# Optimization experiments

Measured on AMD Instinct MI355X. Metric: run time of the kernel, lower is better.

The kernel has to match this reference:

```python
import jax, jax.numpy as jnp
import numpy as np

TOPK = 2  # config.topk_exp


def setup_inputs() -> dict:
    key = jax.random.key(0)
    ks = jax.random.split(key, 4)
    B, S, D, F, E = 4, 1024, 768, 3072, 8
    scale_in = 1.0 / np.sqrt(D)
    scale_hid = 1.0 / np.sqrt(F)
    return {
        "x": jax.random.normal(ks[0], (B, S, D), dtype=jnp.float32),
        "router_w": jax.random.normal(ks[1], (E, D), dtype=jnp.float32) * scale_in,
        "w_fc": jax.random.normal(ks[2], (E, D, F), dtype=jnp.float32) * scale_in,
        "b_fc": jnp.zeros((E, F), dtype=jnp.float32),
        "w_proj": jax.random.normal(ks[3], (E, F, D), dtype=jnp.float32) * scale_hid,
        "b_proj": jnp.zeros((E, D), dtype=jnp.float32),
    }


def _moe_forward(x, router_w, w_fc, b_fc, w_proj, b_proj):
    B, S, D = x.shape
    E = router_w.shape[0]
    xt = x.reshape(-1, D)  # [T, D] tokens
    # per-token router: Linear(D, E, bias=False)
    gate_logits = xt @ router_w.T  # [T, E]
    # topk_exp > 1: raw logits -> topk -> softmax over the k selected logits
    weights, selected = jax.lax.top_k(gate_logits, TOPK)  # [T, k]
    weights = jax.nn.softmax(weights.astype(jnp.float32), axis=1).astype(x.dtype)
    # combine weights per expert: w[t, e] = sum_k weights[t,k] * (selected[t,k]==e)
    onehot = jax.nn.one_hot(selected, E, dtype=x.dtype)  # [T, k, E]
    comb = jnp.einsum('tk,tke->te', weights, onehot)  # [T, E]
    # expert MLP (GPT-2 style: fc -> gelu -> proj), evaluated densely then combined
    h = jax.nn.gelu(jnp.einsum('td,edf->etf', xt, w_fc) + b_fc[:, None, :], approximate=False)
    y = jnp.einsum('etf,efd->etd', h, w_proj) + b_proj[:, None, :]  # [E, T, D]
    out = jnp.einsum('te,etd->td', comb, y)  # weighted scatter-combine
    return out.reshape(B, S, D)


def reference(x, router_w, w_fc, b_fc, w_proj, b_proj):
    return _moe_forward(x, router_w, w_fc, b_fc, w_proj, b_proj)
```

## Files before the change

kernel.cpp:

```cpp
#include <hip/hip_runtime.h>
#include <hip/hip_bf16.h>

#define TT 4096
#define DD 768
#define FF 3072
#define EE 8
#define NSLOT 8192
#define NSLOT_PAD 8448

#define WVM0  0x0F70

typedef __attribute__((ext_vector_type(8))) short bf16x8;
typedef __attribute__((ext_vector_type(4))) float f32x4;
typedef const __attribute__((address_space(1))) void* gas1_t;
typedef __attribute__((address_space(3))) void* las3_t;

__global__ __launch_bounds__(256) void router2_kernel(const float* __restrict__ x,
    const float* __restrict__ rw, int* __restrict__ tokE, float* __restrict__ tokW,
    int* __restrict__ blkCnt) {
  __shared__ float rws[EE * 832];
  __shared__ int cnt_s[EE];
  int tid = threadIdx.x;
  if (tid < EE) cnt_s[tid] = 0;
#pragma unroll
  for (int k = 0; k < 6; ++k) {
    int c = tid + k * 256;
    int e = c / 192, rem = c % 192;
    int s = rem / 12, i = rem % 12;
    float4 v = *(const float4*)&rw[e * DD + s * 48 + i * 4];
    *(float4*)&rws[e * 832 + s * 52 + i * 4] = v;
  }
  __syncthreads();
  int lane = tid & 63;
  int sl = lane & 15;
  int t = blockIdx.x * 16 + (tid >> 6) * 4 + (lane >> 4);
  const float4* xp = (const float4*)(x + (size_t)t * DD + sl * 48);
  float acc[EE];
#pragma unroll
  for (int e = 0; e < EE; ++e) acc[e] = 0.f;
#pragma unroll
  for (int i = 0; i < 12; ++i) {
    float4 xv = xp[i];
#pragma unroll
    for (int e = 0; e < EE; ++e) {
      float4 rv = *(const float4*)&rws[e * 832 + sl * 52 + i * 4];
      acc[e] = fmaf(xv.x, rv.x, fmaf(xv.y, rv.y, fmaf(xv.z, rv.z, fmaf(xv.w, rv.w, acc[e]))));
    }
  }
#pragma unroll
  for (int off = 8; off > 0; off >>= 1) {
#pragma unroll
    for (int e = 0; e < EE; ++e) acc[e] += __shfl_xor(acc[e], off);
  }
  if (sl == 0) {
    float v0 = -1e30f; int e0 = 0;
#pragma unroll
    for (int e = 0; e < EE; ++e) { if (acc[e] > v0) { v0 = acc[e]; e0 = e; } }
    float v1 = -1e30f; int e1 = 0;
#pragma unroll
    for (int e = 0; e < EE; ++e) { if (e != e0 && acc[e] > v1) { v1 = acc[e]; e1 = e; } }
    float w1 = 1.f / (1.f + __expf(v0 - v1));
    float w0 = 1.f - w1;
    tokE[2 * t] = e0; tokE[2 * t + 1] = e1;
    tokW[2 * t] = w0; tokW[2 * t + 1] = w1;
    atomicAdd(&cnt_s[e0], 1);
    atomicAdd(&cnt_s[e1], 1);
  }
  __syncthreads();
  if (tid < EE) blkCnt[blockIdx.x * EE + tid] = cnt_s[tid];
}

__global__ __launch_bounds__(256) void offsets2_kernel(const int* __restrict__ blkCnt,
    int* __restrict__ offs, int* __restrict__ blkBase,
    int* __restrict__ tile1, int* __restrict__ tile2, int* __restrict__ meta) {
  __shared__ int wsum[4][EE];
  int tid = threadIdx.x;
  int lane = tid & 63, w = tid >> 6;
  int c[EE], s[EE];
#pragma unroll
  for (int e = 0; e < EE; ++e) { c[e] = blkCnt[tid * EE + e]; s[e] = c[e]; }
#pragma unroll
  for (int off = 1; off < 64; off <<= 1) {
#pragma unroll
    for (int e = 0; e < EE; ++e) {
      int v = __shfl_up(s[e], off);
      if (lane >= off) s[e] += v;
    }
  }
  if (lane == 63) {
#pragma unroll
    for (int e = 0; e < EE; ++e) wsum[w][e] = s[e];
  }
  __syncthreads();
#pragma unroll
  for (int e = 0; e < EE; ++e) {
    int pre = 0;
    for (int w2 = 0; w2 < w; ++w2) pre += wsum[w2][e];
    s[e] += pre;
  }
  int tot[EE];
#pragma unroll
  for (int e = 0; e < EE; ++e) tot[e] = wsum[0][e] + wsum[1][e] + wsum[2][e] + wsum[3][e];
  int offl[EE + 1];
  offl[0] = 0;
#pragma unroll
  for (int e = 0; e < EE; ++e) offl[e + 1] = offl[e] + tot[e];
#pragma unroll
  for (int e = 0; e < EE; ++e) blkBase[tid * EE + e] = offl[e] + s[e] - c[e];
  if (tid == 0) {
    for (int e = 0; e <= EE; ++e) offs[e] = offl[e];
    int n1 = 0, n2 = 0;
    for (int e = 0; e < EE; ++e) { n1 += (tot[e] + 127) / 128; n2 += (tot[e] + 255) / 256; }
    meta[0] = n1; meta[1] = n2;
  }
  if (tid < EE) {
    int p1 = 0, p2 = 0;
    for (int e = 0; e < tid; ++e) { p1 += (tot[e] + 127) / 128; p2 += (tot[e] + 255) / 256; }
    for (int m = 0; m < tot[tid]; m += 128) tile1[p1++] = (tid << 20) | m;
    for (int m = 0; m < tot[tid]; m += 256) tile2[p2++] = (tid << 20) | m;
  }
}

__global__ __launch_bounds__(256) void scatter_gather2_kernel(const float* __restrict__ x,
    const int* __restrict__ tokE, const float* __restrict__ tokW,
    const int* __restrict__ blkBase, int* __restrict__ slotIdx, float* __restrict__ slotW,
    int* __restrict__ slotTok, __hip_bfloat16* __restrict__ Xg) {
  __shared__ int base_s[EE], lcur[EE];
  __shared__ int sl_s[16][2];
  int tid = threadIdx.x;
  int b = blockIdx.x;
  if (tid < EE) { base_s[tid] = blkBase[b * EE + tid]; lcur[tid] = 0; }
  __syncthreads();
  if (tid < 16) {
    int t = b * 16 + tid;
    int e0 = tokE[2 * t], e1 = tokE[2 * t + 1];
    int s0 = base_s[e0] + atomicAdd(&lcur[e0], 1);
    int s1 = base_s[e1] + atomicAdd(&lcur[e1], 1);
    slotIdx[2 * t] = s0; slotIdx[2 * t + 1] = s1;
    slotW[s0] = tokW[2 * t]; slotW[s1] = tokW[2 * t + 1];
    slotTok[s0] = t; slotTok[s1] = t;
    sl_s[tid][0] = s0; sl_s[tid][1] = s1;
  }
  __syncthreads();
  int k = tid >> 4, p = tid & 15;
  int t = b * 16 + k;
  int s0 = sl_s[k][0], s1 = sl_s[k][1];
  const float4* src = (const float4*)(x + (size_t)t * DD);
  ushort4* d0 = (ushort4*)(Xg + (size_t)s0 * DD);
  ushort4* d1 = (ushort4*)(Xg + (size_t)s1 * DD);
#pragma unroll
  for (int i = 0; i < 12; ++i) {
    int idx = i * 16 + p;
    float4 v = src[idx];
    union { ushort4 u; __hip_bfloat16 h[4]; } cv;
    cv.h[0] = __float2bfloat16(v.x);
    cv.h[1] = __float2bfloat16(v.y);
    cv.h[2] = __float2bfloat16(v.z);
    cv.h[3] = __float2bfloat16(v.w);
    d0[idx] = cv.u;
    d1[idx] = cv.u;
  }
}

__global__ void transpose_convert_kernel(const float* __restrict__ w_fc, __hip_bfloat16* __restrict__ wfcT,
                                         const float* __restrict__ w_proj, __hip_bfloat16* __restrict__ wprojT) {
  __shared__ float tile[64][65];
  int bx = blockIdx.x;
  const float* S; __hip_bfloat16* D; int K, N, n0, k0;
  if (bx < 576) { S = w_fc;   D = wfcT;   K = DD; N = FF; n0 = (bx % 48) * 64; k0 = (bx / 48) * 64; }
  else { bx -= 576; S = w_proj; D = wprojT; K = FF; N = DD; n0 = (bx % 12) * 64; k0 = (bx / 12) * 64; }
  S += (size_t)blockIdx.z * K * N;
  D += (size_t)blockIdx.z * K * N;
  int tid = threadIdx.x;
#pragma unroll
  for (int i = 0; i < 4; ++i) {
    int slot = i * 256 + tid;
    int r = slot >> 4, c4 = slot & 15;
    float4 v = *(const float4*)&S[(size_t)(k0 + r) * N + n0 + c4 * 4];
    tile[r][c4 * 4 + 0] = v.x; tile[r][c4 * 4 + 1] = v.y;
    tile[r][c4 * 4 + 2] = v.z; tile[r][c4 * 4 + 3] = v.w;
  }
  __syncthreads();
#pragma unroll
  for (int i = 0; i < 4; ++i) {
    int slot = i * 256 + tid;
    int n = slot >> 4, kc = slot & 15;
    union { ushort4 u; __hip_bfloat16 h[4]; } cv;
    cv.h[0] = __float2bfloat16(tile[kc * 4 + 0][n]);
    cv.h[1] = __float2bfloat16(tile[kc * 4 + 1][n]);
    cv.h[2] = __float2bfloat16(tile[kc * 4 + 2][n]);
    cv.h[3] = __float2bfloat16(tile[kc * 4 + 3][n]);
    *(ushort4*)&D[(size_t)(n0 + n) * K + k0 + kc * 4] = cv.u;
  }
}

__device__ __forceinline__ float rcp_fast(float x) {
  float r; asm("v_rcp_f32 %0, %1" : "=v"(r) : "v"(x)); return r;
}

__device__ __forceinline__ float gelu_f(float v) {
  float z = v * 0.70710678118654752f;
  float az = fabsf(z);
  float t = rcp_fast(1.0f + 0.3275911f * az);
  float poly = t * (0.254829592f + t * (-0.284496736f + t * (1.421413741f +
               t * (-1.453152027f + t * 1.061405429f))));
  float erf_abs = 1.0f - poly * __expf(-az * az);
  float erf = copysignf(erf_abs, z);
  return 0.5f * v * (1.0f + erf);
}

#define G_ISSUE(NXT) \
  _Pragma("unroll") for (int i = 0; i < 4; ++i) { \
    __builtin_amdgcn_global_load_lds((gas1_t)gA[i], (las3_t)(&As[NXT][0] + fsd[i]), 16, 0, 0); \
    __builtin_amdgcn_global_load_lds((gas1_t)gB[i], (las3_t)(&Bs[NXT][0] + fsd[i]), 16, 0, 0); \
    gA[i] += 64; gB[i] += 64; }

#define G_COMP(CUR) \
  { const short* cA = &As[CUR][0]; const short* cB = &Bs[CUR][0]; \
    _Pragma("unroll") for (int s = 0; s < 2; ++s) { \
      bf16x8 af[4], bfr[4]; \
      _Pragma("unroll") for (int mi = 0; mi < 4; ++mi) af[mi] = *(const bf16x8*)(cA + (aoff[mi] ^ (s * 32))); \
      _Pragma("unroll") for (int ni = 0; ni < 4; ++ni) bfr[ni] = *(const bf16x8*)(cB + (boff[ni] ^ (s * 32))); \
      _Pragma("unroll") for (int mi = 0; mi < 4; ++mi) \
        _Pragma("unroll") for (int ni = 0; ni < 4; ++ni) \
          acc[mi][ni] = __builtin_amdgcn_mfma_f32_16x16x32_bf16(af[mi], bfr[ni], acc[mi][ni], 0, 0, 0); } }

#define S_MAIN(CUR, NXT) \
  __builtin_amdgcn_s_waitcnt(WVM0); \
  __builtin_amdgcn_s_barrier(); \
  G_ISSUE(NXT) \
  G_COMP(CUR)

#define S_LAST(CUR) \
  __builtin_amdgcn_s_waitcnt(WVM0); \
  __builtin_amdgcn_s_barrier(); \
  G_COMP(CUR)

__global__ __launch_bounds__(256) void gemm2_kernel(const __hip_bfloat16* __restrict__ H,
    const __hip_bfloat16* __restrict__ wprojT, const float* __restrict__ b_proj,
    const float* __restrict__ slotW, const int* __restrict__ slotTok,
    float* __restrict__ out, const int* __restrict__ offs,
    const int* __restrict__ tile1, const int* __restrict__ meta) {
  __shared__ __align__(16) short As[2][128 * 64];
  __shared__ __align__(16) short Bs[2][128 * 64];
  int wg = blockIdx.x + 6 * blockIdx.y;
  int wl = (wg & 7) * 54 + (wg >> 3);
  int bx = wl % 6;
  int by = wl / 6;
  if (by >= meta[0]) return;
  int tv = tile1[by];
  int e = tv >> 20;
  int m_base = tv & 0xFFFFF;
  int off_e = offs[e];
  int n_e = offs[e + 1] - off_e;
  int n0 = bx * 128;
  const short* A = (const short*)H + (size_t)(off_e + m_base) * FF;
  const short* B = (const short*)wprojT + (size_t)e * DD * FF + (size_t)n0 * FF;
  int tid = threadIdx.x;
  int lane = tid & 63, wid = tid >> 6;
  int l15 = lane & 15, q = lane >> 4;
  int wm = wid & 1, wn = wid >> 1;
  int fsd[4];
  const short* gA[4];
  const short* gB[4];
#pragma unroll
  for (int i = 0; i < 4; ++i) {
    int fs = tid + i * 256;
    int m = fs >> 3, c = (fs & 7) ^ (m & 7);
    fsd[i] = fs * 8;
    gA[i] = A + (size_t)m * FF + c * 8;
    gB[i] = B + (size_t)m * FF + c * 8;
  }
  int aoff[4], boff[4];
#pragma unroll
  for (int mi = 0; mi < 4; ++mi) {
    int r = wm * 64 + mi * 16 + l15;
    aoff[mi] = r * 64 + ((q ^ (r & 7)) * 8);
  }
#pragma unroll
  for (int ni = 0; ni < 4; ++ni) {
    int r = wn * 64 + ni * 16 + l15;
    boff[ni] = r * 64 + ((q ^ (r & 7)) * 8);
  }
  f32x4 acc[4][4] = {};
  G_ISSUE(0)
  for (int g = 0; g < 23; ++g) {
    S_MAIN(0, 1)
    S_MAIN(1, 0)
  }
  S_MAIN(0, 1)
  S_LAST(1)
  float bias[4];
#pragma unroll
  for (int ni = 0; ni < 4; ++ni)
    bias[ni] = b_proj[e * DD + n0 + wn * 64 + ni * 16 + l15];
#pragma unroll
  for (int mi = 0; mi < 4; ++mi) {
#pragma unroll
    for (int r = 0; r < 4; ++r) {
      int ml = wm * 64 + mi * 16 + q * 4 + r;
      if (m_base + ml < n_e) {
        int slot = off_e + m_base + ml;
        float w = slotW[slot];
        int tok = slotTok[slot];
        float* op = out + (size_t)tok * DD + n0 + wn * 64;
#pragma unroll
        for (int ni = 0; ni < 4; ++ni)
          atomicAdd(&op[ni * 16 + l15], w * (acc[mi][ni][r] + bias[ni]));
      }
    }
  }
}

#define G1_ISSUE(NXT) \
  _Pragma("unroll") for (int i = 0; i < 4; ++i) { \
    __builtin_amdgcn_global_load_lds((gas1_t)gA[i], (las3_t)(&As[NXT][0] + fsd[i]), 16, 0, 0); \
    __builtin_amdgcn_global_load_lds((gas1_t)gB[i], (las3_t)(&Bs[NXT][0] + fsd[i]), 16, 0, 0); \
    gA[i] += 64; gB[i] += 64; }

#define G1_COMP(CUR) \
  { const short* cA = &As[CUR][0]; const short* cB = &Bs[CUR][0]; \
    _Pragma("unroll") for (int s = 0; s < 2; ++s) { \
      bf16x8 af[8], bfr[4]; \
      _Pragma("unroll") for (int mi = 0; mi < 8; ++mi) af[mi] = *(const bf16x8*)(cA + (aoff[mi] ^ (s * 32))); \
      _Pragma("unroll") for (int ni = 0; ni < 4; ++ni) bfr[ni] = *(const bf16x8*)(cB + (boff[ni] ^ (s * 32))); \
      _Pragma("unroll") for (int mi = 0; mi < 8; ++mi) \
        _Pragma("unroll") for (int ni = 0; ni < 4; ++ni) \
          acc[mi][ni] = __builtin_amdgcn_mfma_f32_16x16x32_bf16(af[mi], bfr[ni], acc[mi][ni], 0, 0, 0); } }

#define S1_MAIN(CUR, NXT) \
  __builtin_amdgcn_s_waitcnt(WVM0); \
  __builtin_amdgcn_s_barrier(); \
  G1_ISSUE(NXT) \
  G1_COMP(CUR)

#define S1_LAST(CUR) \
  __builtin_amdgcn_s_waitcnt(WVM0); \
  __builtin_amdgcn_s_barrier(); \
  G1_COMP(CUR)

__global__ __launch_bounds__(512, 2) void gemm1_kernel(const __hip_bfloat16* __restrict__ Xg,
    const __hip_bfloat16* __restrict__ wfcT, const float* __restrict__ b_fc,
    __hip_bfloat16* __restrict__ H, const int* __restrict__ offs,
    const int* __restrict__ tile2, const int* __restrict__ meta) {
  __shared__ __align__(16) short As[2][256 * 64];
  __shared__ __align__(16) short Bs[2][256 * 64];
  int wg = blockIdx.x + 12 * blockIdx.y;
  int wl = (wg & 7) * 60 + (wg >> 3);
  int bx = wl % 12;
  int by = wl / 12;
  if (by >= meta[1]) return;
  int tv = tile2[by];
  int e = tv >> 20;
  int m_base = tv & 0xFFFFF;
  int off_e = offs[e];
  int n_e = offs[e + 1] - off_e;
  int n0 = bx * 256;
  const short* A = (const short*)Xg + (size_t)(off_e + m_base) * DD;
  const short* B = (const short*)wfcT + (size_t)e * FF * DD + (size_t)n0 * DD;
  int tid = threadIdx.x;
  int lane = tid & 63, wid = tid >> 6;
  int l15 = lane & 15, q = lane >> 4;
  int wm = wid & 1, wn = wid >> 1;
  int fsd[4];
  const short* gA[4];
  const short* gB[4];
#pragma unroll
  for (int i = 0; i < 4; ++i) {
    int fs = tid + i * 512;
    int m = fs >> 3, c = (fs & 7) ^ (m & 7);
    fsd[i] = fs * 8;
    gA[i] = A + (size_t)m * DD + c * 8;
    gB[i] = B + (size_t)m * DD + c * 8;
  }
  int aoff[8], boff[4];
#pragma unroll
  for (int mi = 0; mi < 8; ++mi) {
    int r = wm * 128 + mi * 16 + l15;
    aoff[mi] = r * 64 + ((q ^ (r & 7)) * 8);
  }
#pragma unroll
  for (int ni = 0; ni < 4; ++ni) {
    int r = wn * 64 + ni * 16 + l15;
    boff[ni] = r * 64 + ((q ^ (r & 7)) * 8);
  }
  f32x4 acc[8][4] = {};
  G1_ISSUE(0)
  for (int g = 0; g < 5; ++g) {
    S1_MAIN(0, 1)
    S1_MAIN(1, 0)
  }
  S1_MAIN(0, 1)
  S1_LAST(1)
  float bias[4];
#pragma unroll
  for (int ni = 0; ni < 4; ++ni) bias[ni] = b_fc[e * FF + n0 + wn * 64 + ni * 16 + l15];
  __hip_bfloat16* Hp = H + (size_t)(off_e + m_base) * FF + n0;
#pragma unroll
  for (int mi = 0; mi < 8; ++mi) {
#pragma unroll
    for (int r = 0; r < 4; ++r) {
      int ml = wm * 128 + mi * 16 + q * 4 + r;
      if (m_base + ml < n_e) {
#pragma unroll
        for (int ni = 0; ni < 4; ++ni) {
          int nl = wn * 64 + ni * 16 + l15;
          float v = acc[mi][ni][r] + bias[ni];
          Hp[(size_t)ml * FF + nl] = __float2bfloat16(gelu_f(v));
        }
      }
    }
  }
}

extern "C" void kernel_launch(void* const* d_in, const int* in_sizes, int n_in,
                              void* d_out, int out_size, void* d_ws, size_t ws_size,
                              hipStream_t stream) {
  const float* x        = (const float*)d_in[0];
  const float* router_w = (const float*)d_in[1];
  const float* w_fc     = (const float*)d_in[2];
  const float* b_fc     = (const float*)d_in[3];
  const float* w_proj   = (const float*)d_in[4];
  const float* b_proj   = (const float*)d_in[5];
  float* out = (float*)d_out;

  char* p = (char*)d_ws;
  auto alloc = [&](size_t bytes) {
    char* r = p;
    p += (bytes + 255) & ~(size_t)255;
    return r;
  };
  __hip_bfloat16* wfcT   = (__hip_bfloat16*)alloc((size_t)EE * FF * DD * 2);
  __hip_bfloat16* wprojT = (__hip_bfloat16*)alloc((size_t)EE * DD * FF * 2);
  __hip_bfloat16* Xg     = (__hip_bfloat16*)alloc((size_t)NSLOT_PAD * DD * 2);
  __hip_bfloat16* H      = (__hip_bfloat16*)alloc((size_t)NSLOT_PAD * FF * 2);
  int*   tokE    = (int*)alloc(TT * 2 * 4);
  float* tokW    = (float*)alloc(TT * 2 * 4);
  int*   slotIdx = (int*)alloc(TT * 2 * 4);
  float* slotW   = (float*)alloc(NSLOT_PAD * 4);
  int*   slotTok = (int*)alloc(NSLOT_PAD * 4);
  int*   blkCnt  = (int*)alloc(256 * EE * 4);
  int*   blkBase = (int*)alloc(256 * EE * 4);
  int*   tile1   = (int*)alloc(128 * 4);
  int*   tile2   = (int*)alloc(256 * 4);
  int*   offs    = (int*)alloc(64);
  int*   meta    = (int*)alloc(64);

  hipMemsetAsync(out, 0, (size_t)out_size * 4, stream);
  router2_kernel<<<256, 256, 0, stream>>>(x, router_w, tokE, tokW, blkCnt);
  offsets2_kernel<<<1, 256, 0, stream>>>(blkCnt, offs, blkBase, tile1, tile2, meta);
  scatter_gather2_kernel<<<256, 256, 0, stream>>>(x, tokE, tokW, blkBase, slotIdx, slotW, slotTok, Xg);
  transpose_convert_kernel<<<dim3(1152, 1, EE), 256, 0, stream>>>(w_fc, wfcT, w_proj, wprojT);
  gemm1_kernel<<<dim3(12, 40), 512, 0, stream>>>(Xg, wfcT, b_fc, H, offs, tile2, meta);
  gemm2_kernel<<<dim3(6, 72), 256, 0, stream>>>(H, wprojT, b_proj, slotW, slotTok, out, offs, tile1, meta);
}
```

Baseline: 340.8 us.

## Interleave gemm1 global-to-LDS loads with MFMA phases using barriers and priority

Restructures the gemm1 main loop into four sub-phases per K tile. Each phase loads a slice of A/B fragments from LDS and issues part of the next tile's global_load_lds, then runs a 4x4 MFMA block under raised wave priority, with barriers around each phase. The aim is to spread memory issue across compute and coordinate waves so the matrix cores stay busier, in the style of ping-pong scheduling. In exchange it adds barriers per tile and reorders register use, which may add sync overhead or change register pressure.

```diff
diff --git a/kernel.cpp b/kernel.cpp
--- a/kernel.cpp
+++ b/kernel.cpp
@@ -9,6 +9,7 @@
 #define NSLOT_PAD 8448
 
 #define WVM0  0x0F70
+#define WLG0  0xC07F
 
 typedef __attribute__((ext_vector_type(8))) short bf16x8;
 typedef __attribute__((ext_vector_type(4))) float f32x4;
@@ -312,32 +313,58 @@
   }
 }
 
-#define G1_ISSUE(NXT) \
-  _Pragma("unroll") for (int i = 0; i < 4; ++i) { \
-    __builtin_amdgcn_global_load_lds((gas1_t)gA[i], (las3_t)(&As[NXT][0] + fsd[i]), 16, 0, 0); \
-    __builtin_amdgcn_global_load_lds((gas1_t)gB[i], (las3_t)(&Bs[NXT][0] + fsd[i]), 16, 0, 0); \
-    gA[i] += 64; gB[i] += 64; }
-
-#define G1_COMP(CUR) \
-  { const short* cA = &As[CUR][0]; const short* cB = &Bs[CUR][0]; \
-    _Pragma("unroll") for (int s = 0; s < 2; ++s) { \
-      bf16x8 af[8], bfr[4]; \
-      _Pragma("unroll") for (int mi = 0; mi < 8; ++mi) af[mi] = *(const bf16x8*)(cA + (aoff[mi] ^ (s * 32))); \
-      _Pragma("unroll") for (int ni = 0; ni < 4; ++ni) bfr[ni] = *(const bf16x8*)(cB + (boff[ni] ^ (s * 32))); \
-      _Pragma("unroll") for (int mi = 0; mi < 8; ++mi) \
-        _Pragma("unroll") for (int ni = 0; ni < 4; ++ni) \
-          acc[mi][ni] = __builtin_amdgcn_mfma_f32_16x16x32_bf16(af[mi], bfr[ni], acc[mi][ni], 0, 0, 0); } }
-
-#define S1_MAIN(CUR, NXT) \
-  __builtin_amdgcn_s_waitcnt(WVM0); \
+#define GL1(SRC, ARR, NXT, IDX) \
+  __builtin_amdgcn_global_load_lds((gas1_t)(SRC), (las3_t)(&ARR[NXT][0] + fsd[IDX]), 16, 0, 0);
+
+#define PH_SYNC \
   __builtin_amdgcn_s_barrier(); \
-  G1_ISSUE(NXT) \
-  G1_COMP(CUR)
-
-#define S1_LAST(CUR) \
-  __builtin_amdgcn_s_waitcnt(WVM0); \
-  __builtin_amdgcn_s_barrier(); \
-  G1_COMP(CUR)
+  __builtin_amdgcn_s_waitcnt(WLG0); \
+  __builtin_amdgcn_s_setprio(1);
+
+#define PH_END \
+  __builtin_amdgcn_s_setprio(0); \
+  __builtin_amdgcn_s_barrier();
+
+#define TILE1(CUR, NXT, STG) \
+ { const short* cA = &As[CUR][0]; const short* cB = &Bs[CUR][0]; \
+   bf16x8 b0[4], b1[4], afr[4]; \
+    \
+   _Pragma("unroll") for (int i = 0; i < 4; ++i) afr[i] = *(const bf16x8*)(cA + aoff[i]); \
+   _Pragma("unroll") for (int i = 0; i < 4; ++i) b0[i]  = *(const bf16x8*)(cB + boff[i]); \
+   if (STG) { GL1(gA[0], As, NXT, 0) GL1(gA[1], As, NXT, 1) GL1(gB[0], Bs, NXT, 0) } \
+   PH_SYNC \
+   _Pragma("unroll") for (int mi = 0; mi < 4; ++mi) \
+     _Pragma("unroll") for (int ni = 0; ni < 4; ++ni) \
+       acc[mi][ni] = __builtin_amdgcn_mfma_f32_16x16x32_bf16(afr[mi], b0[ni], acc[mi][ni], 0, 0, 0); \
+   PH_END \
+    \
+   _Pragma("unroll") for (int i = 0; i < 4; ++i) afr[i] = *(const bf16x8*)(cA + (aoff[i] ^ 32)); \
+   _Pragma("unroll") for (int i = 0; i < 4; ++i) b1[i]  = *(const bf16x8*)(cB + (boff[i] ^ 32)); \
+   if (STG) { GL1(gA[2], As, NXT, 2) GL1(gA[3], As, NXT, 3) GL1(gB[1], Bs, NXT, 1) } \
+   PH_SYNC \
+   _Pragma("unroll") for (int mi = 0; mi < 4; ++mi) \
+     _Pragma("unroll") for (int ni = 0; ni < 4; ++ni) \
+       acc[mi][ni] = __builtin_amdgcn_mfma_f32_16x16x32_bf16(afr[mi], b1[ni], acc[mi][ni], 0, 0, 0); \
+   PH_END \
+    \
+   _Pragma("unroll") for (int i = 0; i < 4; ++i) afr[i] = *(const bf16x8*)(cA + aoff[4 + i]); \
+   if (STG) { GL1(gB[2], Bs, NXT, 2) GL1(gB[3], Bs, NXT, 3) } \
+   PH_SYNC \
+   _Pragma("unroll") for (int mi = 0; mi < 4; ++mi) \
+     _Pragma("unroll") for (int ni = 0; ni < 4; ++ni) \
+       acc[4 + mi][ni] = __builtin_amdgcn_mfma_f32_16x16x32_bf16(afr[mi], b0[ni], acc[4 + mi][ni], 0, 0, 0); \
+   PH_END \
+    \
+   _Pragma("unroll") for (int i = 0; i < 4; ++i) afr[i] = *(const bf16x8*)(cA + (aoff[4 + i] ^ 32)); \
+   PH_SYNC \
+   _Pragma("unroll") for (int mi = 0; mi < 4; ++mi) \
+     _Pragma("unroll") for (int ni = 0; ni < 4; ++ni) \
+       acc[4 + mi][ni] = __builtin_amdgcn_mfma_f32_16x16x32_bf16(afr[mi], b1[ni], acc[4 + mi][ni], 0, 0, 0); \
+   __builtin_amdgcn_s_setprio(0); \
+   __builtin_amdgcn_s_waitcnt(WVM0); \
+   __builtin_amdgcn_s_barrier(); \
+   if (STG) { _Pragma("unroll") for (int i = 0; i < 4; ++i) { gA[i] += 64; gB[i] += 64; } } \
+ }
 
 __global__ __launch_bounds__(512, 2) void gemm1_kernel(const __hip_bfloat16* __restrict__ Xg,
     const __hip_bfloat16* __restrict__ wfcT, const float* __restrict__ b_fc,
@@ -385,13 +412,16 @@
     boff[ni] = r * 64 + ((q ^ (r & 7)) * 8);
   }
   f32x4 acc[8][4] = {};
-  G1_ISSUE(0)
+#pragma unroll
+  for (int i = 0; i < 4; ++i) { GL1(gA[i], As, 0, i) GL1(gB[i], Bs, 0, i) gA[i] += 64; gB[i] += 64; }
+  __builtin_amdgcn_s_waitcnt(WVM0);
+  __builtin_amdgcn_s_barrier();
   for (int g = 0; g < 5; ++g) {
-    S1_MAIN(0, 1)
-    S1_MAIN(1, 0)
-  }
-  S1_MAIN(0, 1)
-  S1_LAST(1)
+    TILE1(0, 1, 1)
+    TILE1(1, 0, 1)
+  }
+  TILE1(0, 1, 1)
+  TILE1(1, 0, 0)
   float bias[4];
 #pragma unroll
   for (int ni = 0; ni < 4; ++ni) bias[ni] = b_fc[e * FF + n0 + wn * 64 + ni * 16 + l15];
```

After: 344.9 us. About the same (+1.2%).
